# Kernel tuning notes

Measured on AMD Instinct MI355X. Metric: run time of the kernel, lower is better.

The kernel has to match this reference:

```python
import jax, jax.numpy as jnp
import numpy as np

VAR0, VAR1 = 0.1, 0.2
THRESHOLD = 0.35
NEGPOS_RATIO = 7
LOW_GT_THRESH = 0.2  # match() filters GT whose best prior IoU < 0.2


def setup_inputs() -> dict:
    key = jax.random.key(0)
    ks = jax.random.split(key, 8)
    B, P, G = 16, 43008, 128
    loc_data = jax.random.normal(ks[0], (B, P, 4), jnp.float32)
    conf_data = jax.random.normal(ks[1], (B, P, 2), jnp.float32)
    landm_data = jax.random.normal(ks[2], (B, P, 10), jnp.float32)
    # priors in cxcywh form, positive sizes
    pc = jax.random.uniform(ks[3], (P, 2), jnp.float32)
    pwh = jax.random.uniform(ks[4], (P, 2), jnp.float32, minval=0.02, maxval=0.32)
    priors = jnp.concatenate([pc, pwh], axis=1)
    # targets: valid xyxy boxes + 10 landmark coords + label (face=1)
    ctr = jax.random.uniform(ks[5], (B, G, 2), jnp.float32, minval=0.2, maxval=0.8)
    wh = jax.random.uniform(ks[6], (B, G, 2), jnp.float32, minval=0.05, maxval=0.3)
    boxes = jnp.concatenate([ctr - wh / 2, ctr + wh / 2], axis=-1)
    landms = jax.random.uniform(ks[7], (B, G, 10), jnp.float32)
    labels = jnp.ones((B, G, 1), jnp.float32)
    targets = jnp.concatenate([boxes, landms, labels], axis=-1)
    return {"loc_data": loc_data, "conf_data": conf_data, "landm_data": landm_data,
            "priors": priors, "targets": targets}


def point_form(priors):
    return jnp.concatenate([priors[:, :2] - priors[:, 2:] / 2,
                            priors[:, :2] + priors[:, 2:] / 2], axis=1)


def jaccard(a, b):  # a: [G,4] xyxy, b: [P,4] xyxy -> [G,P]
    lt = jnp.maximum(a[:, None, :2], b[None, :, :2])
    rb = jnp.minimum(a[:, None, 2:], b[None, :, 2:])
    wh = jnp.clip(rb - lt, 0.0)
    inter = wh[..., 0] * wh[..., 1]
    area_a = (a[:, 2] - a[:, 0]) * (a[:, 3] - a[:, 1])
    area_b = (b[:, 2] - b[:, 0]) * (b[:, 3] - b[:, 1])
    return inter / (area_a[:, None] + area_b[None, :] - inter)


def encode(matched, priors):  # matched xyxy [P,4], priors cxcywh [P,4]
    g_cxcy = (matched[:, :2] + matched[:, 2:]) / 2 - priors[:, :2]
    g_cxcy = g_cxcy / (VAR0 * priors[:, 2:])
    g_wh = jnp.log((matched[:, 2:] - matched[:, :2]) / priors[:, 2:]) / VAR1
    return jnp.concatenate([g_cxcy, g_wh], axis=1)


def encode_landm(matched, priors):  # matched [P,10], priors [P,4]
    m = matched.reshape(-1, 5, 2)
    g = (m - priors[:, None, :2]) / (VAR0 * priors[:, None, 2:])
    return g.reshape(-1, 10)


def match_one(truths, labels, landms, priors):
    G = truths.shape[0]
    overlaps = jaccard(truths, point_form(priors))  # [G, P]
    best_prior_overlap = overlaps.max(axis=1)       # [G]
    best_prior_idx = overlaps.argmax(axis=1)        # [G]
    valid = best_prior_overlap >= LOW_GT_THRESH
    any_valid = jnp.any(valid)
    best_truth_overlap = overlaps.max(axis=0)       # [P]
    best_truth_idx = overlaps.argmax(axis=0)        # [P]
    # index_fill_(0, best_prior_idx_filter, 2): ensure each valid GT keeps its best prior
    fill_val = jnp.where(valid, 2.0, best_truth_overlap[best_prior_idx])
    best_truth_overlap = best_truth_overlap.at[best_prior_idx].set(fill_val)
    # best_truth_idx[best_prior_idx[j]] = j for all j
    best_truth_idx = best_truth_idx.at[best_prior_idx].set(jnp.arange(G))
    matches = truths[best_truth_idx]                       # [P,4]
    conf = labels[best_truth_idx].astype(jnp.int32)        # [P]
    conf = jnp.where(best_truth_overlap < THRESHOLD, 0, conf)
    conf = jnp.where(any_valid, conf, 0)  # no valid GT -> all background
    loc = encode(matches, priors)
    landm = encode_landm(landms[best_truth_idx], priors)
    return loc, conf, landm


def smooth_l1(x):
    ax = jnp.abs(x)
    return jnp.where(ax < 1.0, 0.5 * ax * ax, ax - 0.5)


def reference(loc_data, conf_data, landm_data, priors, targets):
    truths = targets[..., :4]
    landms = targets[..., 4:14]
    labels = targets[..., 14]
    loc_t, conf_t, landm_t = jax.vmap(
        lambda t, l, lm: match_one(t, l, lm, priors))(truths, labels, landms)

    # landmark loss over positives
    pos1 = conf_t > 0
    N1 = jnp.maximum(pos1.sum().astype(jnp.float32), 1.0)
    loss_landm = jnp.sum(smooth_l1(landm_data - landm_t) * pos1[..., None])

    # localization loss over positives
    pos = conf_t != 0
    num_pos = pos.sum(axis=1, keepdims=True)  # [B,1]
    loss_l = jnp.sum(smooth_l1(loc_data - loc_t) * pos[..., None])

    # hard negative mining on per-prior CE loss
    lse = jax.scipy.special.logsumexp(conf_data, axis=-1)  # [B,P]
    gathered = jnp.take_along_axis(conf_data, conf_t[..., None], axis=-1)[..., 0]
    ce_all = lse - gathered                                # [B,P] per-prior CE
    mine = jnp.where(pos, 0.0, ce_all)
    loss_idx = jnp.argsort(-mine, axis=1)
    idx_rank = jnp.argsort(loss_idx, axis=1)
    num_neg = jnp.clip(NEGPOS_RATIO * num_pos, None, pos.shape[1] - 1)
    neg = idx_rank < num_neg
    sel = pos | neg
    loss_c = jnp.sum(jnp.where(sel, ce_all, 0.0))

    N = jnp.maximum(num_pos.sum().astype(jnp.float32), 1.0)
    return loss_l / N, loss_c / N, loss_landm / N1
```

## Files before the change

kernel.cpp:

```cpp
#include <hip/hip_runtime.h>
#include <stdint.h>


#define GC 8
#define PPI 4

__device__ __forceinline__ float sl1(float x) {
  float a = fabsf(x);
  return a < 1.f ? 0.5f * a * a : a - 0.5f;
}

__device__ __forceinline__ double dwave(double v) {
#pragma unroll
  for (int o = 32; o; o >>= 1) v += __shfl_down(v, o);
  return v;
}

__device__ __forceinline__ unsigned bsufscan(unsigned x, unsigned* S,
                                             unsigned* wt, int tid) {
  int lane = tid & 63, wid = tid >> 6;
  unsigned v = x;
#pragma unroll
  for (int o = 1; o < 64; o <<= 1) {
    unsigned u = __shfl_down(v, o);
    if (lane + o < 64) v += u;
  }
  if (lane == 0) wt[wid] = v;
  __syncthreads();
  if (wid == 0) {
    unsigned tv = (lane < 16) ? wt[lane] : 0;
#pragma unroll
    for (int o = 1; o < 16; o <<= 1) {
      unsigned u = __shfl_down(tv, o);
      if (lane + o < 64) tv += u;
    }
    if (lane < 16) wt[lane] = tv;
  }
  __syncthreads();
  unsigned Sv = v + ((wid < 15) ? wt[wid + 1] : 0u);
  S[tid] = Sv;
  __syncthreads();
  return Sv;
}

__global__ __launch_bounds__(256) void k_mm(
    const float* __restrict__ priors, const float* __restrict__ targets,
    const float* __restrict__ loc, const float* __restrict__ conf,
    const float* __restrict__ lm, float* __restrict__ bto,
    int* __restrict__ bti, unsigned long long* __restrict__ bp,
    float* __restrict__ mine, unsigned* __restrict__ ghist,
    double* __restrict__ pll, double* __restrict__ pllm,
    double* __restrict__ plc, double* __restrict__ msum,
    int* __restrict__ pnp, int P, int G, int NIOU, int PTI, int NGC, int PC) {
  int tid = threadIdx.x;
  __shared__ char smem[16384];
  __shared__ float4 sgt[128];
  __shared__ float sga[128];

  if ((int)blockIdx.x < NIOU) {
    float* st = (float*)smem;
    double* rs = (double*)(smem + 7680);
    int* ri = (int*)(smem + 7808);
    unsigned* hist = (unsigned*)(smem + 8192);
    int b = blockIdx.x / PTI, tile = blockIdx.x % PTI;
    int base = tile * (256 * PPI);
    for (int i = tid; i < G * 15; i += 256)
      st[i] = targets[(size_t)b * G * 15 + i];
    for (int g = tid; g < G; g += 256) {
      const float* t = targets + ((size_t)b * G + g) * 15;
      float x1 = t[0], y1 = t[1], x2 = t[2], y2 = t[3];
      sgt[g] = make_float4(x1, y1, x2, y2);
      sga[g] = (x2 - x1) * (y2 - y1);
    }
    for (int i = tid; i < 1024; i += 256) hist[i] = 0;
    __syncthreads();

    float px1[PPI], py1[PPI], px2[PPI], py2[PPI], pa[PPI];
    float bi[PPI], sb[PPI];
    int bidx[PPI];
#pragma unroll
    for (int k = 0; k < PPI; ++k) {
      int p = base + tid + k * 256;
      int pl = p < P ? p : P - 1;
      float4 pr = ((const float4*)priors)[pl];
      px1[k] = pr.x - pr.z * 0.5f; py1[k] = pr.y - pr.w * 0.5f;
      px2[k] = pr.x + pr.z * 0.5f; py2[k] = pr.y + pr.w * 0.5f;
      pa[k] = pr.z * pr.w;
      bi[k] = 0.f; sb[k] = 1.f; bidx[k] = 0;
    }

#define IOU_BODY(T, A, GG)                                                 \
  {                                                                        \
    float iw = fminf(T.z, px2[k]) - fmaxf(T.x, px1[k]);                    \
    float ih = fminf(T.w, py2[k]) - fmaxf(T.y, py1[k]);                    \
    float inter = fmaxf(iw, 0.f) * ih;                                     \
    float S = A + pa[k];                                                   \
    if (inter * sb[k] > bi[k] * S) { bi[k] = inter; sb[k] = S; bidx[k] = GG; } \
  }
    for (int g = 0; g < G; g += 4) {
      float4 T0 = sgt[g], T1 = sgt[g + 1], T2 = sgt[g + 2], T3 = sgt[g + 3];
      float A0 = sga[g], A1 = sga[g + 1], A2 = sga[g + 2], A3 = sga[g + 3];
#pragma unroll
      for (int k = 0; k < PPI; ++k) {
        IOU_BODY(T0, A0, g)
        IOU_BODY(T1, A1, g + 1)
        IOU_BODY(T2, A2, g + 2)
        IOU_BODY(T3, A3, g + 3)
      }
    }
#undef IOU_BODY

    double ll = 0, llm = 0, lc = 0, ms = 0;
    int np = 0;
#pragma unroll
    for (int k = 0; k < PPI; ++k) {
      int p = base + tid + k * 256;
      if (p < P) {
        size_t idx = (size_t)b * P + p;
        float ov = bi[k] / (sb[k] - bi[k]);
        int ti = bidx[k];
        bto[idx] = ov;
        bti[idx] = ti;
        bool pos = ov >= 0.35f;
        float2 c = ((const float2*)conf)[idx];
        float mx = fmaxf(c.x, c.y);
        float dd = fabsf(c.x - c.y);
        float lse = mx + logf(1.f + expf(-dd));
        float ce = lse - (pos ? c.y : c.x);
        float mv = pos ? 0.f : ce;
        mine[idx] = mv;
        atomicAdd(&hist[__float_as_uint(mv) >> 21], 1u);
        ms += (double)mv;
        if (pos) {
          np++;
          lc += (double)ce;
          float4 pr = ((const float4*)priors)[p];
          const float* t = st + ti * 15;
          float rz = 1.f / pr.z, rw = 1.f / pr.w;
          float rdx = 10.f * rz, rdy = 10.f * rw;
          float gx = ((t[0] + t[2]) * 0.5f - pr.x) * rdx;
          float gy = ((t[1] + t[3]) * 0.5f - pr.y) * rdy;
          float gw = logf((t[2] - t[0]) * rz) * 5.0f;
          float gh = logf((t[3] - t[1]) * rw) * 5.0f;
          float4 ld = ((const float4*)loc)[idx];
          ll += (double)(sl1(ld.x - gx) + sl1(ld.y - gy) + sl1(ld.z - gw) +
                         sl1(ld.w - gh));
          const float2* lmd = (const float2*)lm + idx * 5;
          float s = 0.f;
#pragma unroll
          for (int j = 0; j < 5; ++j) {
            float2 lv = lmd[j];
            float ex = (t[4 + 2 * j] - pr.x) * rdx;
            float ey = (t[5 + 2 * j] - pr.y) * rdy;
            s += sl1(lv.x - ex) + sl1(lv.y - ey);
          }
          llm += (double)s;
        }
      }
    }

    ll = dwave(ll); llm = dwave(llm); lc = dwave(lc); ms = dwave(ms);
#pragma unroll
    for (int o = 32; o; o >>= 1) np += __shfl_down(np, o);
    int lane = tid & 63, wid = tid >> 6;
    if (lane == 0) {
      rs[wid] = ll; rs[4 + wid] = llm; rs[8 + wid] = lc; rs[12 + wid] = ms;
      ri[wid] = np;
    }
    __syncthreads();
    if (tid == 0) {
      pll[blockIdx.x] = rs[0] + rs[1] + rs[2] + rs[3];
      pllm[blockIdx.x] = rs[4] + rs[5] + rs[6] + rs[7];
      plc[blockIdx.x] = rs[8] + rs[9] + rs[10] + rs[11];
      msum[blockIdx.x] = rs[12] + rs[13] + rs[14] + rs[15];
      pnp[blockIdx.x] = ri[0] + ri[1] + ri[2] + ri[3];
    }
    for (int i = tid; i < 1024; i += 256) {
      unsigned c = hist[i];
      if (c) atomicAdd(&ghist[b * 1024 + i], c);
    }
  } else {
    unsigned long long* sred = (unsigned long long*)smem;
    int bc = blockIdx.x - NIOU;
    int pc = bc % PC;
    int gcb = (bc / PC) % NGC;
    int b = bc / (PC * NGC);
    int g0 = gcb * GC;

    if (tid < GC) {
      int g = g0 + tid;
      float4 v = make_float4(0.f, 0.f, 0.f, 0.f);
      if (g < G) {
        const float* t = targets + ((size_t)b * G + g) * 15;
        v = make_float4(t[0], t[1], t[2], t[3]);
      }
      sgt[tid] = v;
    }
    __syncthreads();

    float gx1[GC], gy1[GC], gx2[GC], gy2[GC], ga[GC];
#pragma unroll
    for (int j = 0; j < GC; ++j) {
      float4 T = sgt[j];
      gx1[j] = T.x; gy1[j] = T.y; gx2[j] = T.z; gy2[j] = T.w;
      ga[j] = (T.z - T.x) * (T.w - T.y);
    }

    int chunk = (P + PC - 1) / PC;
    int ps = pc * chunk;
    int pe = ps + chunk; if (pe > P) pe = P;
    int count = pe - ps;

    float bi[GC], sb[GC];
    unsigned bpp[GC];
#pragma unroll
    for (int j = 0; j < GC; ++j) { bi[j] = 0.f; sb[j] = 1.f; bpp[j] = (unsigned)(ps + tid); }

#define BP_BODY(X1, Y1, X2, Y2, AR, PP)                                     \
  {                                                                         \
    float iw = fminf(gx2[j], X2) - fmaxf(gx1[j], X1);                       \
    float ih = fminf(gy2[j], Y2) - fmaxf(gy1[j], Y1);                       \
    float inter = fmaxf(iw, 0.f) * ih;                                      \
    float S = ga[j] + AR;                                                   \
    if (inter * sb[j] > bi[j] * S) { bi[j] = inter; sb[j] = S; bpp[j] = (unsigned)PP; } \
  }
    for (int i = tid; i < count; i += 1024) {
      int p0 = ps + i;
      int i1 = i + 256, i2 = i + 512, i3 = i + 768;
      int p1 = (i1 < count) ? ps + i1 : p0;
      int p2 = (i2 < count) ? ps + i2 : p0;
      int p3 = (i3 < count) ? ps + i3 : p0;
      float4 q0 = ((const float4*)priors)[p0];
      float4 q1 = ((const float4*)priors)[p1];
      float4 q2 = ((const float4*)priors)[p2];
      float4 q3 = ((const float4*)priors)[p3];
      float ax1 = q0.x - q0.z * 0.5f, ay1 = q0.y - q0.w * 0.5f;
      float ax2 = q0.x + q0.z * 0.5f, ay2 = q0.y + q0.w * 0.5f;
      float aa = q0.z * q0.w;
      float bx1 = q1.x - q1.z * 0.5f, by1 = q1.y - q1.w * 0.5f;
      float bx2 = q1.x + q1.z * 0.5f, by2 = q1.y + q1.w * 0.5f;
      float ba = q1.z * q1.w;
      float cx1 = q2.x - q2.z * 0.5f, cy1 = q2.y - q2.w * 0.5f;
      float cx2 = q2.x + q2.z * 0.5f, cy2 = q2.y + q2.w * 0.5f;
      float ca = q2.z * q2.w;
      float dx1 = q3.x - q3.z * 0.5f, dy1 = q3.y - q3.w * 0.5f;
      float dx2 = q3.x + q3.z * 0.5f, dy2 = q3.y + q3.w * 0.5f;
      float da = q3.z * q3.w;
#pragma unroll
      for (int j = 0; j < GC; ++j) {
        BP_BODY(ax1, ay1, ax2, ay2, aa, p0)
        BP_BODY(bx1, by1, bx2, by2, ba, p1)
        BP_BODY(cx1, cy1, cx2, cy2, ca, p2)
        BP_BODY(dx1, dy1, dx2, dy2, da, p3)
      }
    }
#undef BP_BODY

#pragma unroll
    for (int j = 0; j < GC; ++j) {
      float iou = bi[j] / (sb[j] - bi[j]);
      unsigned long long pk =
          ((unsigned long long)__float_as_uint(iou) << 32) | (unsigned)(~bpp[j]);
      sred[j * 256 + tid] = pk;
    }
    __syncthreads();
    {
      int j = tid >> 5, s = tid & 31;
      unsigned long long m = sred[j * 256 + s];
#pragma unroll
      for (int t = 1; t < 8; ++t) {
        unsigned long long v = sred[j * 256 + s + t * 32];
        if (v > m) m = v;
      }
      __syncthreads();
      sred[j * 256 + s] = m;
    }
    __syncthreads();
    if (tid < GC) {
      unsigned long long m = sred[tid * 256];
      for (int s = 1; s < 32; ++s) {
        unsigned long long v = sred[tid * 256 + s];
        if (v > m) m = v;
      }
      int g = g0 + tid;
      if (g < G) atomicMax(&bp[(size_t)b * G + g], m);
    }
  }
}

__global__ __launch_bounds__(1024) void k_tail2(
    const unsigned long long* __restrict__ bp, float* __restrict__ bto,
    const int* __restrict__ bti, const float* __restrict__ conf,
    const float* __restrict__ loc, const float* __restrict__ lm,
    const float* __restrict__ priors, const float* __restrict__ targets,
    float* __restrict__ mine, unsigned* __restrict__ ghist,
    const int* __restrict__ pnp, const double* __restrict__ msum,
    const double* __restrict__ pll, const double* __restrict__ pllm,
    const double* __restrict__ plc, double* __restrict__ gacc,
    int* __restrict__ gnp, unsigned* __restrict__ done,
    float* __restrict__ out, int P, int G, int PTI, int B) {
  int b = blockIdx.x, tid = threadIdx.x;
  int lane = tid & 63, wid = tid >> 6;
  __shared__ unsigned spp[128];
  __shared__ double rs[16 * 5];
  __shared__ int ris[16];
  __shared__ unsigned S[1024];
  __shared__ unsigned hs[2048];
  __shared__ unsigned wt[16];
  __shared__ double sdel[4];
  __shared__ int sdnp, sav, smode;
  __shared__ long long sk;
  __shared__ double sA, sC, sD;
  __shared__ int snpos;
  __shared__ int st_, sk1_;
  __shared__ unsigned lcnt;
  __shared__ int spf21, sk2;
  __shared__ unsigned stb;
  __shared__ double stie;

  double dll = 0, dllm = 0, dlc = 0, dms = 0;
  int dnp = 0;
  unsigned pp = 0;
  bool valid = false;
  if (tid < G) {
    unsigned long long m = bp[(size_t)b * G + tid];
    pp = ~(unsigned)m;
    float val = __uint_as_float((unsigned)(m >> 32));
    spp[tid] = pp;
    valid = val >= 0.2f;
  }
  int av = __syncthreads_or((tid < G && valid) ? 1 : 0);
  bool win = false;
  if (tid < G) {
    win = true;
    for (int g2 = tid + 1; g2 < G; ++g2)
      if (spp[g2] == pp) { win = false; break; }
  }
  if (win) {
    size_t idx = (size_t)b * P + pp;
    float ov_o = bto[idx];
    int ti_o = bti[idx];
    float ov_n = valid ? 2.0f : ov_o;
    int ti_n = tid;
    bool pos_o = ov_o >= 0.35f, pos_n = ov_n >= 0.35f;

    float2 c = ((const float2*)conf)[idx];
    float mx = fmaxf(c.x, c.y);
    float dd = fabsf(c.x - c.y);
    float lse = mx + logf(1.f + expf(-dd));
    float ce_o = lse - (pos_o ? c.y : c.x);
    float ce_n = lse - (pos_n ? c.y : c.x);
    float mv_o = mine[idx];
    float mv_n = pos_n ? 0.f : ce_n;
    if (mv_n != mv_o) {
      mine[idx] = mv_n;
      atomicSub(&ghist[b * 1024 + (__float_as_uint(mv_o) >> 21)], 1u);
      atomicAdd(&ghist[b * 1024 + (__float_as_uint(mv_n) >> 21)], 1u);
    }
    dms = (double)mv_n - (double)mv_o;
    dnp = (pos_n ? 1 : 0) - (pos_o ? 1 : 0);
    dlc = (pos_n ? (double)ce_n : 0.0) - (pos_o ? (double)ce_o : 0.0);

    if (pos_o || pos_n) {
      float4 pr = ((const float4*)priors)[pp];
      float rz = 1.f / pr.z, rw = 1.f / pr.w;
      float rdx = 10.f * rz, rdy = 10.f * rw;
      float4 ld = ((const float4*)loc)[idx];
      const float2* lmd = (const float2*)lm + idx * 5;
      float2 lv[5];
#pragma unroll
      for (int j = 0; j < 5; ++j) lv[j] = lmd[j];
      for (int pass = 0; pass < 2; ++pass) {
        bool act = pass ? pos_n : pos_o;
        int ti = pass ? ti_n : ti_o;
        if (!act) continue;
        const float* t = targets + ((size_t)b * G + ti) * 15;
        float gx = ((t[0] + t[2]) * 0.5f - pr.x) * rdx;
        float gy = ((t[1] + t[3]) * 0.5f - pr.y) * rdy;
        float gw = logf((t[2] - t[0]) * rz) * 5.0f;
        float gh = logf((t[3] - t[1]) * rw) * 5.0f;
        double l = (double)(sl1(ld.x - gx) + sl1(ld.y - gy) +
                            sl1(ld.z - gw) + sl1(ld.w - gh));
        float s = 0.f;
#pragma unroll
        for (int j = 0; j < 5; ++j) {
          float ex = (t[4 + 2 * j] - pr.x) * rdx;
          float ey = (t[5 + 2 * j] - pr.y) * rdy;
          s += sl1(lv[j].x - ex) + sl1(lv[j].y - ey);
        }
        if (pass) { dll += l; dllm += (double)s; }
        else { dll -= l; dllm -= (double)s; }
      }
    }
  }
  dll = dwave(dll); dllm = dwave(dllm); dlc = dwave(dlc); dms = dwave(dms);
#pragma unroll
  for (int o = 32; o; o >>= 1) dnp += __shfl_down(dnp, o);
  if (lane == 0) {
    rs[wid] = dll; rs[16 + wid] = dllm; rs[32 + wid] = dlc; rs[48 + wid] = dms;
    ris[wid] = dnp;
  }
  __syncthreads();
  if (tid == 0) {
    double a = 0, c2 = 0, d2 = 0, m2 = 0;
    int n2 = 0;
    for (int i = 0; i < 16; ++i) {
      a += rs[i]; c2 += rs[16 + i]; d2 += rs[32 + i]; m2 += rs[48 + i];
      n2 += ris[i];
    }
    sdel[0] = a; sdel[1] = c2; sdel[2] = d2; sdel[3] = m2;
    sdnp = n2; sav = av;
  }
  __syncthreads();

  double a = 0, cc = 0, d = 0, ms = 0;
  int n = 0;
  for (int i = tid; i < PTI; i += 1024) {
    int ix = b * PTI + i;
    a += pll[ix]; cc += pllm[ix]; d += plc[ix]; ms += msum[ix]; n += pnp[ix];
  }
  a = dwave(a); cc = dwave(cc); d = dwave(d); ms = dwave(ms);
#pragma unroll
  for (int o = 32; o; o >>= 1) n += __shfl_down(n, o);
  if (lane == 0) {
    rs[wid] = a; rs[16 + wid] = cc; rs[32 + wid] = d; rs[48 + wid] = ms;
    ris[wid] = n;
  }
  __syncthreads();
  double Fv = 0.0;
  if (tid == 0) {
    double A = 0, C = 0, D = 0, MS = 0;
    int npos = 0;
    for (int i = 0; i < 16; ++i) {
      A += rs[i]; C += rs[16 + i]; D += rs[32 + i]; MS += rs[48 + i];
      npos += ris[i];
    }
    A += sdel[0]; C += sdel[1]; D += sdel[2]; MS += sdel[3];
    npos += sdnp;
    if (!sav) { A = 0; C = 0; D = 0; npos = 0; }
    sA = A; sC = C; sD = D; snpos = npos;
    long long k = 7LL * (long long)npos;
    long long cap = P - 1;
    int md = 1;
    if (k <= 0) { Fv = 0.0; md = 0; }
    else if (k >= cap) { Fv = MS; md = 0; }
    smode = md; sk = k;
  }
  __syncthreads();

  if (smode) {
    long long k = sk;
    {
      unsigned x = ghist[b * 1024 + tid];
      unsigned Sv = bsufscan(x, S, wt, tid);
      int cnt_ = __syncthreads_count((long long)Sv >= k);
      int seg = cnt_ - 1;
      if (tid == seg) {
        long long cum = (seg + 1 < 1024) ? (long long)S[seg + 1] : 0;
        st_ = seg;
        sk1_ = (int)(k - cum);
      }
      if (tid == 0) lcnt = 0;
    }
    __syncthreads();
    int t = st_;
    long long k1 = (long long)sk1_;

    const float* mrow = mine + (size_t)b * P;
    float* crow = bto + (size_t)b * P;
    double acc = 0;
    for (int base0 = 0; base0 < P; base0 += 4096) {
#pragma unroll
      for (int j = 0; j < 4; ++j) {
        int p = base0 + tid + j * 1024;
        if (p < P) {
          unsigned bb = __float_as_uint(mrow[p]);
          int bin = (int)(bb >> 21);
          if (bin > t) acc += (double)__uint_as_float(bb);
          else if (bin == t) {
            unsigned pos = atomicAdd(&lcnt, 1u);
            crow[pos] = __uint_as_float(bb);
          }
        }
      }
    }
    acc = dwave(acc);
    if (lane == 0) rs[wid] = acc;
    __syncthreads();
    int nn = (int)lcnt;

    hs[tid] = 0; hs[tid + 1024] = 0;
    __syncthreads();
    for (int i = tid; i < nn; i += 1024) {
      unsigned bb = __float_as_uint(crow[i]);
      atomicAdd(&hs[(bb >> 10) & 2047], 1u);
    }
    __syncthreads();
    {
      unsigned h0 = hs[tid * 2], h1v = hs[tid * 2 + 1];
      unsigned Sv = bsufscan(h0 + h1v, S, wt, tid);
      int cnt_ = __syncthreads_count((long long)Sv >= k1);
      int seg = cnt_ - 1;
      if (tid == seg) {
        long long cum = (seg + 1 < 1024) ? (long long)S[seg + 1] : 0;
        int bin = seg * 2;
        if (cum + h1v >= k1) bin = seg * 2 + 1;
        else cum += h1v;
        spf21 = (t << 11) | bin;
        sk2 = (int)(k1 - cum);
      }
    }
    __syncthreads();
    int pf21 = spf21;

    hs[tid] = 0;
    __syncthreads();
    for (int i = tid; i < nn; i += 1024) {
      unsigned bb = __float_as_uint(crow[i]);
      if ((int)(bb >> 10) == pf21) atomicAdd(&hs[bb & 1023], 1u);
    }
    __syncthreads();
    {
      unsigned Sv = bsufscan(hs[tid], S, wt, tid);
      long long kk = (long long)sk2;
      int cnt_ = __syncthreads_count((long long)Sv >= kk);
      int seg = cnt_ - 1;
      if (tid == seg) {
        long long cum = (seg + 1 < 1024) ? (long long)S[seg + 1] : 0;
        unsigned tb = ((unsigned)pf21 << 10) | (unsigned)seg;
        stb = tb;
        stie = (double)(kk - cum) * (double)__uint_as_float(tb);
      }
    }
    __syncthreads();

    unsigned tb = stb;
    double v = 0.0;
    for (int i = tid; i < nn; i += 1024) {
      unsigned bb = __float_as_uint(crow[i]);
      if (bb > tb) v += (double)__uint_as_float(bb);
    }
    v = dwave(v);
    if (lane == 0) rs[16 + wid] = v;
    __syncthreads();
    if (tid == 0) {
      double hi = 0, vt = 0;
      for (int i = 0; i < 16; ++i) { hi += rs[i]; vt += rs[16 + i]; }
      Fv = hi + vt + stie;
    }
  }

  if (tid == 0) {
    atomicAdd(&gacc[0], sA);
    atomicAdd(&gacc[1], sC);
    atomicAdd(&gacc[2], sD);
    atomicAdd(&gacc[3], Fv);
    atomicAdd(gnp, snpos);
    __threadfence();
    unsigned old = atomicAdd(done, 1u);
    if (old == (unsigned)B - 1) {
      __threadfence();
      double A = atomicAdd(&gacc[0], 0.0);
      double C = atomicAdd(&gacc[1], 0.0);
      double D = atomicAdd(&gacc[2], 0.0);
      double F = atomicAdd(&gacc[3], 0.0);
      int N = atomicAdd(gnp, 0);
      double Nd = N < 1 ? 1.0 : (double)N;
      out[0] = (float)(A / Nd);
      out[1] = (float)((D + F) / Nd);
      out[2] = (float)(C / Nd);
    }
  }
}

extern "C" void kernel_launch(void* const* d_in, const int* in_sizes, int n_in,
                              void* d_out, int out_size, void* d_ws,
                              size_t ws_size, hipStream_t stream) {
  const float* loc = (const float*)d_in[0];
  const float* conf = (const float*)d_in[1];
  const float* lm = (const float*)d_in[2];
  const float* priors = (const float*)d_in[3];
  const float* targets = (const float*)d_in[4];

  int P = in_sizes[3] / 4;
  int B = in_sizes[0] / (4 * P);
  int G = in_sizes[4] / (15 * B);
  int PTI = (P + 256 * PPI - 1) / (256 * PPI);
  int NIOU = B * PTI;
  int NGC = (G + GC - 1) / GC;
  int PC = 8;
  int NBP = B * NGC * PC;

  char* w = (char*)d_ws;
  size_t off = 0;
  unsigned long long* bp = (unsigned long long*)(w + off);
  off += (size_t)B * G * 8;
  unsigned* ghist = (unsigned*)(w + off);
  off += (size_t)B * 1024 * 4;
  double* gacc = (double*)(w + off);
  off += 4 * 8;
  int* gnp = (int*)(w + off);
  off += 4;
  unsigned* done = (unsigned*)(w + off);
  off += 4;
  size_t clear_bytes = off;
  off = (off + 255) & ~(size_t)255;
  float* bto = (float*)(w + off);
  off += (size_t)B * P * 4;
  int* bti = (int*)(w + off);
  off += (size_t)B * P * 4;
  float* mine = (float*)(w + off);
  off += (size_t)B * P * 4;
  double* pll = (double*)(w + off);
  off += (size_t)NIOU * 8;
  double* pllm = (double*)(w + off);
  off += (size_t)NIOU * 8;
  double* plc = (double*)(w + off);
  off += (size_t)NIOU * 8;
  double* msum = (double*)(w + off);
  off += (size_t)NIOU * 8;
  int* pnp = (int*)(w + off);
  off += (size_t)NIOU * 4;

  hipMemsetAsync(d_ws, 0, clear_bytes, stream);

  k_mm<<<NIOU + NBP, 256, 0, stream>>>(priors, targets, loc, conf, lm, bto,
                                       bti, bp, mine, ghist, pll, pllm, plc,
                                       msum, pnp, P, G, NIOU, PTI, NGC, PC);
  k_tail2<<<B, 1024, 0, stream>>>(bp, bto, bti, conf, loc, lm, priors,
                                  targets, mine, ghist, pnp, msum, pll, pllm,
                                  plc, gacc, gnp, done, (float*)d_out, P, G,
                                  PTI, B);
}
```

Before: 179.2 us.

## Spatially bin priors and skip IoU work for non-overlapping wavefront bounding boxes

Adds a pre-pass that buckets priors into a 16x16 grid by center and by size class, scatters them into sorted order, and computes a per-64-prior bounding box. The matching kernels then compare each ground-truth box against that wavefront-uniform bbox and skip the IoU math when the two cannot overlap. Original prior indices are carried along through sid so results are written in original order. The cost is four extra small kernel launches, an atomic-based scatter that is nondeterministic within a cell, and changed tie-breaking for equal IoU. Tie-breaking now depends on the sorted order, and the bp==0 case is handled specially.

```diff
diff --git a/kernel.cpp b/kernel.cpp
--- a/kernel.cpp
+++ b/kernel.cpp
@@ -4,6 +4,7 @@
 
 #define GC 8
 #define PPI 4
+#define NCELL 1024
 
 __device__ __forceinline__ float sl1(float x) {
   float a = fabsf(x);
@@ -14,6 +15,18 @@
 #pragma unroll
   for (int o = 32; o; o >>= 1) v += __shfl_down(v, o);
   return v;
+}
+
+__device__ __forceinline__ unsigned fflip(float f) {
+  unsigned u = __float_as_uint(f);
+  return (u & 0x80000000u) ? ~u : (u | 0x80000000u);
+}
+
+__device__ __forceinline__ int cellOf(float4 pr) {
+  int cx = (int)(pr.x * 16.f); cx = cx < 0 ? 0 : (cx > 15 ? 15 : cx);
+  int cy = (int)(pr.y * 16.f); cy = cy < 0 ? 0 : (cy > 15 ? 15 : cy);
+  return ((cy * 16 + cx) << 2) | ((pr.z > 0.17f) ? 2 : 0) |
+         ((pr.w > 0.17f) ? 1 : 0);
 }
 
 __device__ __forceinline__ unsigned bsufscan(unsigned x, unsigned* S,
@@ -43,8 +56,67 @@
   return Sv;
 }
 
+__global__ __launch_bounds__(256) void k_hist(const float* __restrict__ priors,
+                                              unsigned* __restrict__ cellh,
+                                              int P) {
+  int p = blockIdx.x * 256 + threadIdx.x;
+  if (p < P) {
+    float4 pr = ((const float4*)priors)[p];
+    atomicAdd(&cellh[cellOf(pr)], 1u);
+  }
+}
+
+__global__ __launch_bounds__(1024) void k_scan(const unsigned* __restrict__ cellh,
+                                               unsigned* __restrict__ cellcur) {
+  int tid = threadIdx.x;
+  __shared__ unsigned s[NCELL];
+  unsigned v = cellh[tid];
+  s[tid] = v;
+  __syncthreads();
+  for (int off = 1; off < NCELL; off <<= 1) {
+    unsigned a = (tid >= off) ? s[tid - off] : 0u;
+    __syncthreads();
+    s[tid] += a;
+    __syncthreads();
+  }
+  cellcur[tid] = s[tid] - v;
+}
+
+__global__ __launch_bounds__(256) void k_scatter(
+    const float* __restrict__ priors, unsigned* __restrict__ cellcur,
+    float4* __restrict__ spr, unsigned* __restrict__ sid, int P) {
+  int p = blockIdx.x * 256 + threadIdx.x;
+  if (p < P) {
+    float4 pr = ((const float4*)priors)[p];
+    unsigned pos = atomicAdd(&cellcur[cellOf(pr)], 1u);
+    spr[pos] = pr;
+    sid[pos] = (unsigned)p;
+  }
+}
+
+__global__ __launch_bounds__(64) void k_wbox(const float4* __restrict__ spr,
+                                             uint4* __restrict__ wboxG, int P) {
+  int p = blockIdx.x * 64 + threadIdx.x;
+  float x1 = 1e30f, y1 = 1e30f, x2 = -1e30f, y2 = -1e30f;
+  if (p < P) {
+    float4 pr = spr[p];
+    x1 = pr.x - pr.z * 0.5f; y1 = pr.y - pr.w * 0.5f;
+    x2 = pr.x + pr.z * 0.5f; y2 = pr.y + pr.w * 0.5f;
+  }
+#pragma unroll
+  for (int o = 32; o; o >>= 1) {
+    x1 = fminf(x1, __shfl_down(x1, o));
+    y1 = fminf(y1, __shfl_down(y1, o));
+    x2 = fmaxf(x2, __shfl_down(x2, o));
+    y2 = fmaxf(y2, __shfl_down(y2, o));
+  }
+  if (threadIdx.x == 0)
+    wboxG[blockIdx.x] = make_uint4(fflip(x1), fflip(y1), fflip(x2), fflip(y2));
+}
+
 __global__ __launch_bounds__(256) void k_mm(
-    const float* __restrict__ priors, const float* __restrict__ targets,
+    const float4* __restrict__ spr, const unsigned* __restrict__ sid,
+    const uint4* __restrict__ wboxG, const float* __restrict__ targets,
     const float* __restrict__ loc, const float* __restrict__ conf,
     const float* __restrict__ lm, float* __restrict__ bto,
     int* __restrict__ bti, unsigned long long* __restrict__ bp,
@@ -56,6 +128,7 @@
   __shared__ char smem[16384];
   __shared__ float4 sgt[128];
   __shared__ float sga[128];
+  __shared__ uint4 sgtI[128];
 
   if ((int)blockIdx.x < NIOU) {
     float* st = (float*)smem;
@@ -71,6 +144,7 @@
       float x1 = t[0], y1 = t[1], x2 = t[2], y2 = t[3];
       sgt[g] = make_float4(x1, y1, x2, y2);
       sga[g] = (x2 - x1) * (y2 - y1);
+      sgtI[g] = make_uint4(fflip(x1), fflip(y1), fflip(x2), fflip(y2));
     }
     for (int i = tid; i < 1024; i += 256) hist[i] = 0;
     __syncthreads();
@@ -82,33 +156,46 @@
     for (int k = 0; k < PPI; ++k) {
       int p = base + tid + k * 256;
       int pl = p < P ? p : P - 1;
-      float4 pr = ((const float4*)priors)[pl];
+      float4 pr = spr[pl];
       px1[k] = pr.x - pr.z * 0.5f; py1[k] = pr.y - pr.w * 0.5f;
       px2[k] = pr.x + pr.z * 0.5f; py2[k] = pr.y + pr.w * 0.5f;
       pa[k] = pr.z * pr.w;
       bi[k] = 0.f; sb[k] = 1.f; bidx[k] = 0;
     }
 
-#define IOU_BODY(T, A, GG)                                                 \
-  {                                                                        \
-    float iw = fminf(T.z, px2[k]) - fmaxf(T.x, px1[k]);                    \
-    float ih = fminf(T.w, py2[k]) - fmaxf(T.y, py1[k]);                    \
-    float inter = fmaxf(iw, 0.f) * ih;                                     \
-    float S = A + pa[k];                                                   \
-    if (inter * sb[k] > bi[k] * S) { bi[k] = inter; sb[k] = S; bidx[k] = GG; } \
-  }
-    for (int g = 0; g < G; g += 4) {
-      float4 T0 = sgt[g], T1 = sgt[g + 1], T2 = sgt[g + 2], T3 = sgt[g + 3];
-      float A0 = sga[g], A1 = sga[g + 1], A2 = sga[g + 2], A3 = sga[g + 3];
+    unsigned wrx1[PPI], wry1[PPI], wrx2[PPI], wry2[PPI];
+    {
+      int wvid = tid >> 6;
 #pragma unroll
       for (int k = 0; k < PPI; ++k) {
-        IOU_BODY(T0, A0, g)
-        IOU_BODY(T1, A1, g + 1)
-        IOU_BODY(T2, A2, g + 2)
-        IOU_BODY(T3, A3, g + 3)
-      }
-    }
-#undef IOU_BODY
+        int run = (base >> 6) + k * 4 + wvid;
+        uint4 wb = wboxG[run];
+        wrx1[k] = (unsigned)__builtin_amdgcn_readfirstlane((int)wb.x);
+        wry1[k] = (unsigned)__builtin_amdgcn_readfirstlane((int)wb.y);
+        wrx2[k] = (unsigned)__builtin_amdgcn_readfirstlane((int)wb.z);
+        wry2[k] = (unsigned)__builtin_amdgcn_readfirstlane((int)wb.w);
+      }
+    }
+
+    for (int g = 0; g < G; ++g) {
+      uint4 gi = sgtI[g];
+      unsigned gx1 = (unsigned)__builtin_amdgcn_readfirstlane((int)gi.x);
+      unsigned gy1 = (unsigned)__builtin_amdgcn_readfirstlane((int)gi.y);
+      unsigned gx2 = (unsigned)__builtin_amdgcn_readfirstlane((int)gi.z);
+      unsigned gy2 = (unsigned)__builtin_amdgcn_readfirstlane((int)gi.w);
+      float4 T = sgt[g];
+      float A = sga[g];
+#pragma unroll
+      for (int k = 0; k < PPI; ++k) {
+        if (gx1 < wrx2[k] && wrx1[k] < gx2 && gy1 < wry2[k] && wry1[k] < gy2) {
+          float iw = fminf(T.z, px2[k]) - fmaxf(T.x, px1[k]);
+          float ih = fminf(T.w, py2[k]) - fmaxf(T.y, py1[k]);
+          float inter = fmaxf(iw, 0.f) * ih;
+          float S = A + pa[k];
+          if (inter * sb[k] > bi[k] * S) { bi[k] = inter; sb[k] = S; bidx[k] = g; }
+        }
+      }
+    }
 
     double ll = 0, llm = 0, lc = 0, ms = 0;
     int np = 0;
@@ -116,7 +203,8 @@
     for (int k = 0; k < PPI; ++k) {
       int p = base + tid + k * 256;
       if (p < P) {
-        size_t idx = (size_t)b * P + p;
+        unsigned op = sid[p];
+        size_t idx = (size_t)b * P + op;
         float ov = bi[k] / (sb[k] - bi[k]);
         int ti = bidx[k];
         bto[idx] = ov;
@@ -134,7 +222,7 @@
         if (pos) {
           np++;
           lc += (double)ce;
-          float4 pr = ((const float4*)priors)[p];
+          float4 pr = spr[p];
           const float* t = st + ti * 15;
           float rz = 1.f / pr.z, rw = 1.f / pr.w;
           float rdx = 10.f * rz, rdy = 10.f * rw;
@@ -205,6 +293,14 @@
       gx1[j] = T.x; gy1[j] = T.y; gx2[j] = T.z; gy2[j] = T.w;
       ga[j] = (T.z - T.x) * (T.w - T.y);
     }
+    unsigned gix1[GC], giy1[GC], gix2[GC], giy2[GC];
+#pragma unroll
+    for (int j = 0; j < GC; ++j) {
+      gix1[j] = (unsigned)__builtin_amdgcn_readfirstlane((int)fflip(gx1[j]));
+      giy1[j] = (unsigned)__builtin_amdgcn_readfirstlane((int)fflip(gy1[j]));
+      gix2[j] = (unsigned)__builtin_amdgcn_readfirstlane((int)fflip(gx2[j]));
+      giy2[j] = (unsigned)__builtin_amdgcn_readfirstlane((int)fflip(gy2[j]));
+    }
 
     int chunk = (P + PC - 1) / PC;
     int ps = pc * chunk;
@@ -214,7 +310,7 @@
     float bi[GC], sb[GC];
     unsigned bpp[GC];
 #pragma unroll
-    for (int j = 0; j < GC; ++j) { bi[j] = 0.f; sb[j] = 1.f; bpp[j] = (unsigned)(ps + tid); }
+    for (int j = 0; j < GC; ++j) { bi[j] = 0.f; sb[j] = 1.f; bpp[j] = 0xFFFFFFFFu; }
 
 #define BP_BODY(X1, Y1, X2, Y2, AR, PP)                                     \
   {                                                                         \
@@ -222,18 +318,20 @@
     float ih = fminf(gy2[j], Y2) - fmaxf(gy1[j], Y1);                       \
     float inter = fmaxf(iw, 0.f) * ih;                                      \
     float S = ga[j] + AR;                                                   \
-    if (inter * sb[j] > bi[j] * S) { bi[j] = inter; sb[j] = S; bpp[j] = (unsigned)PP; } \
+    if (inter * sb[j] > bi[j] * S) { bi[j] = inter; sb[j] = S; bpp[j] = (PP); } \
   }
     for (int i = tid; i < count; i += 1024) {
+      int ib = __builtin_amdgcn_readfirstlane(i);
       int p0 = ps + i;
       int i1 = i + 256, i2 = i + 512, i3 = i + 768;
       int p1 = (i1 < count) ? ps + i1 : p0;
       int p2 = (i2 < count) ? ps + i2 : p0;
       int p3 = (i3 < count) ? ps + i3 : p0;
-      float4 q0 = ((const float4*)priors)[p0];
-      float4 q1 = ((const float4*)priors)[p1];
-      float4 q2 = ((const float4*)priors)[p2];
-      float4 q3 = ((const float4*)priors)[p3];
+      float4 q0 = spr[p0];
+      float4 q1 = spr[p1];
+      float4 q2 = spr[p2];
+      float4 q3 = spr[p3];
+      unsigned s0 = sid[p0], s1 = sid[p1], s2 = sid[p2], s3 = sid[p3];
       float ax1 = q0.x - q0.z * 0.5f, ay1 = q0.y - q0.w * 0.5f;
       float ax2 = q0.x + q0.z * 0.5f, ay2 = q0.y + q0.w * 0.5f;
       float aa = q0.z * q0.w;
@@ -246,12 +344,30 @@
       float dx1 = q3.x - q3.z * 0.5f, dy1 = q3.y - q3.w * 0.5f;
       float dx2 = q3.x + q3.z * 0.5f, dy2 = q3.y + q3.w * 0.5f;
       float da = q3.z * q3.w;
+      unsigned rbx1[4], rby1[4], rbx2[4], rby2[4];
+#pragma unroll
+      for (int q = 0; q < 4; ++q) {
+        int io = ib + q * 256;
+        if (io + 63 < count) {
+          uint4 wb = wboxG[(ps + io) >> 6];
+          rbx1[q] = (unsigned)__builtin_amdgcn_readfirstlane((int)wb.x);
+          rby1[q] = (unsigned)__builtin_amdgcn_readfirstlane((int)wb.y);
+          rbx2[q] = (unsigned)__builtin_amdgcn_readfirstlane((int)wb.z);
+          rby2[q] = (unsigned)__builtin_amdgcn_readfirstlane((int)wb.w);
+        } else {
+          rbx1[q] = 0u; rby1[q] = 0u; rbx2[q] = 0xFFFFFFFFu; rby2[q] = 0xFFFFFFFFu;
+        }
+      }
 #pragma unroll
       for (int j = 0; j < GC; ++j) {
-        BP_BODY(ax1, ay1, ax2, ay2, aa, p0)
-        BP_BODY(bx1, by1, bx2, by2, ba, p1)
-        BP_BODY(cx1, cy1, cx2, cy2, ca, p2)
-        BP_BODY(dx1, dy1, dx2, dy2, da, p3)
+        if (gix1[j] < rbx2[0] && rbx1[0] < gix2[j] && giy1[j] < rby2[0] && rby1[0] < giy2[j])
+          BP_BODY(ax1, ay1, ax2, ay2, aa, s0)
+        if (gix1[j] < rbx2[1] && rbx1[1] < gix2[j] && giy1[j] < rby2[1] && rby1[1] < giy2[j])
+          BP_BODY(bx1, by1, bx2, by2, ba, s1)
+        if (gix1[j] < rbx2[2] && rbx1[2] < gix2[j] && giy1[j] < rby2[2] && rby1[2] < giy2[j])
+          BP_BODY(cx1, cy1, cx2, cy2, ca, s2)
+        if (gix1[j] < rbx2[3] && rbx1[3] < gix2[j] && giy1[j] < rby2[3] && rby1[3] < giy2[j])
+          BP_BODY(dx1, dy1, dx2, dy2, da, s3)
       }
     }
 #undef BP_BODY
@@ -324,7 +440,7 @@
   bool valid = false;
   if (tid < G) {
     unsigned long long m = bp[(size_t)b * G + tid];
-    pp = ~(unsigned)m;
+    pp = (m == 0ull) ? 0u : ~(unsigned)m;
     float val = __uint_as_float((unsigned)(m >> 32));
     spp[tid] = pp;
     valid = val >= 0.2f;
@@ -590,6 +706,8 @@
   int NGC = (G + GC - 1) / GC;
   int PC = 8;
   int NBP = B * NGC * PC;
+  int NPB = (P + 255) / 256;
+  int NRW = PTI * 16;
 
   char* w = (char*)d_ws;
   size_t off = 0;
@@ -597,6 +715,8 @@
   off += (size_t)B * G * 8;
   unsigned* ghist = (unsigned*)(w + off);
   off += (size_t)B * 1024 * 4;
+  unsigned* cellh = (unsigned*)(w + off);
+  off += (size_t)NCELL * 4;
   double* gacc = (double*)(w + off);
   off += 4 * 8;
   int* gnp = (int*)(w + off);
@@ -604,6 +724,15 @@
   unsigned* done = (unsigned*)(w + off);
   off += 4;
   size_t clear_bytes = off;
+  off = (off + 255) & ~(size_t)255;
+  float4* spr = (float4*)(w + off);
+  off += (size_t)NRW * 64 * 16;
+  unsigned* sid = (unsigned*)(w + off);
+  off += (size_t)P * 4;
+  uint4* wboxG = (uint4*)(w + off);
+  off += (size_t)NRW * 16;
+  unsigned* cellcur = (unsigned*)(w + off);
+  off += (size_t)NCELL * 4;
   off = (off + 255) & ~(size_t)255;
   float* bto = (float*)(w + off);
   off += (size_t)B * P * 4;
@@ -624,9 +753,14 @@
 
   hipMemsetAsync(d_ws, 0, clear_bytes, stream);
 
-  k_mm<<<NIOU + NBP, 256, 0, stream>>>(priors, targets, loc, conf, lm, bto,
-                                       bti, bp, mine, ghist, pll, pllm, plc,
-                                       msum, pnp, P, G, NIOU, PTI, NGC, PC);
+  k_hist<<<NPB, 256, 0, stream>>>(priors, cellh, P);
+  k_scan<<<1, 1024, 0, stream>>>(cellh, cellcur);
+  k_scatter<<<NPB, 256, 0, stream>>>(priors, cellcur, spr, sid, P);
+  k_wbox<<<NRW, 64, 0, stream>>>(spr, wboxG, P);
+  k_mm<<<NIOU + NBP, 256, 0, stream>>>(spr, sid, wboxG, targets, loc, conf,
+                                       lm, bto, bti, bp, mine, ghist, pll,
+                                       pllm, plc, msum, pnp, P, G, NIOU, PTI,
+                                       NGC, PC);
   k_tail2<<<B, 1024, 0, stream>>>(bp, bto, bti, conf, loc, lm, priors,
                                   targets, mine, ghist, pnp, msum, pll, pllm,
                                   plc, gacc, gnp, done, (float*)d_out, P, G,
```

Result: slower. 247.3 us (+38.0%).
